# Performance work log

Hardware: AMD Instinct MI355X
Metric: run time of the kernel (lower is better)

## Reference

```python
import jax, jax.numpy as jnp
import numpy as np

B, CIN, COUT, H, W = 2, 256, 256, 96, 96
K, PAD, G = 3, 1, 4           # kernel, padding, deformable_groups
KK = K * K
CG = CIN // G                 # channels per deformable group


def setup_inputs() -> dict:
    key = jax.random.key(0)
    k1, k2, k3, k4 = jax.random.split(key, 4)
    feature = jax.random.normal(k1, (B, CIN, H, W), jnp.float32)
    pred_shape = jax.random.normal(k2, (B, H * W, 4), jnp.float32)
    # init_weights: normal(std=0.01), no biases
    w_offset = jax.random.normal(k3, (G * KK * 2, 4, 1, 1), jnp.float32) * 0.01
    w_deform = jax.random.normal(k4, (COUT, CIN, K, K), jnp.float32) * 0.01
    return {"feature": feature, "pred_shape": pred_shape,
            "w_offset": w_offset, "w_deform": w_deform}


def reference(feature, pred_shape, w_offset, w_deform):
    # pred_shape: (B, H*W, 4) -> (B, 4, H, W); detached in the original
    ps = jnp.transpose(pred_shape, (0, 2, 1)).reshape(B, -1, H, W)
    ps = jax.lax.stop_gradient(ps)
    # 1x1 offset conv: (B, G*2*KK, H, W)
    offset = jnp.einsum('bchw,oc->bohw', ps, w_offset[:, :, 0, 0])
    # mmcv layout per group: [y_k0, x_k0, y_k1, x_k1, ...]
    off = offset.reshape(B, G, KK, 2, H, W)
    off_y, off_x = off[:, :, :, 0], off[:, :, :, 1]   # (B, G, KK, H, W)

    kk = jnp.arange(KK)
    ky = (kk // K).reshape(KK, 1, 1).astype(jnp.float32)
    kx = (kk % K).reshape(KK, 1, 1).astype(jnp.float32)
    yy = jnp.arange(H, dtype=jnp.float32).reshape(1, H, 1)
    xx = jnp.arange(W, dtype=jnp.float32).reshape(1, 1, W)
    # sampling positions (stride=1, dilation=1): (B, G, KK, H, W)
    py = (yy - PAD + ky)[None, None] + off_y
    px = (xx - PAD + kx)[None, None] + off_x

    img = feature.reshape(B, G, CG, H * W)

    def gather(yi, xi):
        # zero outside the image (matches DCN bilinear with zero padding)
        valid = ((yi >= 0) & (yi < H) & (xi >= 0) & (xi < W)).astype(feature.dtype)
        idx = jnp.clip(yi, 0, H - 1) * W + jnp.clip(xi, 0, W - 1)
        v = jnp.take_along_axis(img, idx.reshape(B, G, 1, KK * H * W), axis=3)
        return v.reshape(B, G, CG, KK, H, W) * valid[:, :, None]

    y0 = jnp.floor(py); x0 = jnp.floor(px)
    ly = py - y0; lx = px - x0
    y0i = y0.astype(jnp.int32); x0i = x0.astype(jnp.int32)

    val = ((1 - ly) * (1 - lx))[:, :, None] * gather(y0i, x0i) \
        + ((1 - ly) * lx)[:, :, None] * gather(y0i, x0i + 1) \
        + (ly * (1 - lx))[:, :, None] * gather(y0i + 1, x0i) \
        + (ly * lx)[:, :, None] * gather(y0i + 1, x0i + 1)

    sampled = val.reshape(B, CIN, KK, H, W)
    out = jnp.einsum('bckhw,ock->bohw', sampled, w_deform.reshape(COUT, CIN, KK))
    return jax.nn.relu(out)
```

## Files before the change

### kernel.cpp

```cpp
#include <hip/hip_runtime.h>
#include <hip/hip_bf16.h>
#include <stdint.h>

#define HH   96
#define WW   96
#define HW   9216
#define CIN  256
#define COUT 256
#define NB   2
#define NG   4
#define CG   64
#define KK   9
#define KTOT 2304
#define KB   288
#define TS   8
#define WIN  12
#define W2   13
#define SCH  32

typedef __attribute__((ext_vector_type(8))) short short8;
typedef __attribute__((ext_vector_type(4))) float f32x4;
typedef __attribute__((ext_vector_type(4))) uint32_t u32x4;

__device__ __forceinline__ uint32_t pk2bf(float v0, float v1) {
    __hip_bfloat162 h = __float22bfloat162_rn(make_float2(v0, v1));
    uint32_t u;
    __builtin_memcpy(&u, &h, 4);
    return u;
}

__global__ __launch_bounds__(256) void prep_A(const float* __restrict__ wd,
                                              uint16_t* __restrict__ Ablk) {
    int t  = blockIdx.x * 256 + threadIdx.x;
    int kb = t % KB;
    int o  = t / KB;
    int kkA = kb >> 5;
    int c0A = (kb & 31) * 8;
    const float* src = wd + (size_t)o * KTOT + c0A * KK + kkA;
    float a[8];
#pragma unroll
    for (int e = 0; e < 8; ++e) a[e] = src[e * KK];
    uint16_t* dst = Ablk + ((size_t)kb * 256 + o) * 8;
    u32x4 v;
    v.x = pk2bf(a[0], a[1]);
    v.y = pk2bf(a[2], a[3]);
    v.z = pk2bf(a[4], a[5]);
    v.w = pk2bf(a[6], a[7]);
    *(u32x4*)dst = v;
}

__global__ __launch_bounds__(256) void sampler(const float* __restrict__ feature,
                                               const float* __restrict__ pred,
                                               const float* __restrict__ woff,
                                               uint16_t* __restrict__ S) {
    __shared__ float2 ft2[(SCH / 2) * WIN * W2];

    int tid = threadIdx.x;
    int cb = blockIdx.y, b = blockIdx.z;
    int ch0 = cb * SCH;
    int g = ch0 >> 6;
    int ty = blockIdx.x / (WW / TS), tx = blockIdx.x % (WW / TS);
    int r0 = ty * TS, c0 = tx * TS;
    int rlo = min(max(r0 - 2, 0), HH - WIN);
    int clo = min(max(c0 - 2, 0), WW - WIN);
    bool interior = (rlo >= 1) && (rlo + WIN <= HH - 1) &&
                    (clo >= 1) && (clo + WIN <= WW - 1);

    float* ftf = (float*)ft2;
    const float* fg = feature + ((size_t)(b * CIN + ch0)) * HW;
    for (int e = tid; e < SCH * WIN * WIN; e += 256) {
        int ch = e / (WIN * WIN);
        int re = e - ch * (WIN * WIN);
        int rr = re / WIN, cc = re - rr * WIN;
        ftf[(ch >> 1) * (WIN * W2 * 2) + (rr * W2 + cc) * 2 + (ch & 1)] =
            fg[(size_t)ch * HW + (rlo + rr) * WW + clo + cc];
    }
    __syncthreads();

    int lane = tid & 63, wv = tid >> 6;
    int lr = lane >> 3, lc = lane & 7;
    int hy = r0 + lr, hx = c0 + lc;
    int p = hy * WW + hx;
    float4 ps4 = *(const float4*)(pred + ((size_t)b * HW + p) * 4);

    const float2* ftw = ft2 + (wv * 4) * (WIN * W2);
    const float* fgw = fg + (size_t)(wv * 8) * HW;
    int kb_base = cb * 4 + wv;

#pragma unroll
    for (int kk = 0; kk < KK; ++kk) {
        const float* wy = woff + (g * KK + kk) * 8;
        float offy = ps4.x * wy[0] + ps4.y * wy[1] + ps4.z * wy[2] + ps4.w * wy[3];
        float offx = ps4.x * wy[4] + ps4.y * wy[5] + ps4.z * wy[6] + ps4.w * wy[7];
        float py = (float)(hy - 1 + kk / 3) + offy;
        float px = (float)(hx - 1 + kk % 3) + offx;
        float fy = floorf(py), fx = floorf(px);
        int y0 = (int)fy, x0 = (int)fx;
        float ly = py - fy, lx = px - fx;

        uint16_t* Sp = S + (((size_t)b * KB + (kk * 32 + kb_base)) * HW + p) * 8;
        uint32_t pk[4];

        float c00, c01, c10, c11;
        bool fast;
        int r, q;
        if (interior) {
            fast = (y0 >= rlo) & (y0 <= rlo + WIN - 2) &
                   (x0 >= clo) & (x0 <= clo + WIN - 2);
            if (fast) {
                c00 = (1.f - ly) * (1.f - lx); c01 = (1.f - ly) * lx;
                c10 = ly * (1.f - lx);         c11 = ly * lx;
                r = y0; q = x0;
            } else {
                r = min(max(y0, 0), HH - 2);
                q = min(max(x0, 0), WW - 2);
                float wyA = (y0 == r) ? (1.f - ly) : ((y0 == -1) ? ly : 0.f);
                float wyB = (y0 == r) ? ly : ((y0 == HH - 1) ? (1.f - ly) : 0.f);
                float wxA = (x0 == q) ? (1.f - lx) : ((x0 == -1) ? lx : 0.f);
                float wxB = (x0 == q) ? lx : ((x0 == WW - 1) ? (1.f - lx) : 0.f);
                c00 = wyA * wxA; c01 = wyA * wxB;
                c10 = wyB * wxA; c11 = wyB * wxB;
            }
        } else {
            r = min(max(y0, 0), HH - 2);
            q = min(max(x0, 0), WW - 2);
            float wyA = (y0 == r) ? (1.f - ly) : ((y0 == -1) ? ly : 0.f);
            float wyB = (y0 == r) ? ly : ((y0 == HH - 1) ? (1.f - ly) : 0.f);
            float wxA = (x0 == q) ? (1.f - lx) : ((x0 == -1) ? lx : 0.f);
            float wxB = (x0 == q) ? lx : ((x0 == WW - 1) ? (1.f - lx) : 0.f);
            c00 = wyA * wxA; c01 = wyA * wxB;
            c10 = wyB * wxA; c11 = wyB * wxB;
            fast = (r >= rlo) & (r <= rlo + WIN - 2) &
                   (q >= clo) & (q <= clo + WIN - 2);
        }

        if (fast) {
            int base = (r - rlo) * W2 + (q - clo);
#pragma unroll
            for (int ep = 0; ep < 4; ++ep) {
                const float2* f0 = ftw + ep * (WIN * W2) + base;
                float2 p00 = f0[0], p01 = f0[1];
                float2 p10 = f0[W2], p11 = f0[W2 + 1];
                float v0 = c00 * p00.x + c01 * p01.x + c10 * p10.x + c11 * p11.x;
                float v1 = c00 * p00.y + c01 * p01.y + c10 * p10.y + c11 * p11.y;
                pk[ep] = pk2bf(v0, v1);
            }
        } else {
            size_t gb = (size_t)r * WW + q;
#pragma unroll
            for (int ep = 0; ep < 4; ++ep) {
                const float* f0 = fgw + (size_t)(2 * ep) * HW + gb;
                const float* f1 = f0 + HW;
                float v0 = c00 * f0[0] + c01 * f0[1] + c10 * f0[WW] + c11 * f0[WW + 1];
                float v1 = c00 * f1[0] + c01 * f1[1] + c10 * f1[WW] + c11 * f1[WW + 1];
                pk[ep] = pk2bf(v0, v1);
            }
        }
        u32x4 vv = {pk[0], pk[1], pk[2], pk[3]};
        *(u32x4*)(Sp) = vv;
    }
}

__global__ __launch_bounds__(64, 2) void gemm_kernel(const uint16_t* __restrict__ S,
                                                     const uint16_t* __restrict__ Ablk,
                                                     float* __restrict__ out) {
    int lane = threadIdx.x;
    int bid = blockIdx.x;
    int xcd = bid & 7;
    int j   = bid >> 3;
    int my  = j & 3;
    int pairid = xcd * 36 + (j >> 2);
    int b  = pairid / 144;
    int py = pairid % 144;
    int o0 = my * 64, col0 = py * 64;
    int kc = lane >> 4, il = lane & 15;

    const uint16_t* Ap = Ablk + ((size_t)kc * 256 + o0 + il) * 8;
    const uint16_t* Bp = S + (size_t)b * KB * HW * 8 + ((size_t)kc * HW + col0 + il) * 8;
    const size_t Astep = (size_t)4 * 256 * 8;
    const size_t Bstep = (size_t)4 * HW * 8;

    f32x4 acc[4][4];
#pragma unroll
    for (int m = 0; m < 4; ++m)
#pragma unroll
        for (int n = 0; n < 4; ++n) acc[m][n] = (f32x4){0.f, 0.f, 0.f, 0.f};

    const int NT = KTOT / 32;

    short8 a0[4], b0[4], a1[4], b1[4];

#define LOADT(t, areg, breg)                                                   \
    {                                                                          \
        const uint16_t* ap = Ap + (size_t)(t) * Astep;                         \
        const uint16_t* bp = Bp + (size_t)(t) * Bstep;                         \
        areg[0] = *(const short8*)(ap + 0 * 16 * 8);                           \
        areg[1] = *(const short8*)(ap + 1 * 16 * 8);                           \
        areg[2] = *(const short8*)(ap + 2 * 16 * 8);                           \
        areg[3] = *(const short8*)(ap + 3 * 16 * 8);                           \
        breg[0] = *(const short8*)(bp + 0 * 16 * 8);                           \
        breg[1] = *(const short8*)(bp + 1 * 16 * 8);                           \
        breg[2] = *(const short8*)(bp + 2 * 16 * 8);                           \
        breg[3] = *(const short8*)(bp + 3 * 16 * 8);                           \
    }

#define MFMAT(areg, breg)                                                      \
    {                                                                          \
        _Pragma("unroll")                                                      \
        for (int m = 0; m < 4; ++m)                                            \
            _Pragma("unroll")                                                  \
            for (int n = 0; n < 4; ++n)                                        \
                acc[m][n] = __builtin_amdgcn_mfma_f32_16x16x32_bf16(           \
                    areg[m], breg[n], acc[m][n], 0, 0, 0);                     \
    }

    LOADT(0, a0, b0);
    LOADT(1, a1, b1);

    for (int tt = 0; tt < NT; tt += 2) {
        MFMAT(a0, b0);
        if (tt + 2 < NT) LOADT(tt + 2, a0, b0);
        MFMAT(a1, b1);
        if (tt + 3 < NT) LOADT(tt + 3, a1, b1);
    }
#undef LOADT
#undef MFMAT

    int r4 = kc * 4;
    size_t obase = ((size_t)b * COUT + o0) * HW + col0;
#pragma unroll
    for (int m = 0; m < 4; ++m)
#pragma unroll
        for (int n = 0; n < 4; ++n)
#pragma unroll
            for (int r = 0; r < 4; ++r) {
                float v = acc[m][n][r];
                v = v > 0.f ? v : 0.f;
                out[obase + (size_t)(m * 16 + r4 + r) * HW + n * 16 + il] = v;
            }
}

extern "C" void kernel_launch(void* const* d_in, const int* in_sizes, int n_in,
                              void* d_out, int out_size, void* d_ws, size_t ws_size,
                              hipStream_t stream) {
    (void)in_sizes; (void)n_in; (void)out_size; (void)ws_size;
    const float* feature = (const float*)d_in[0];
    const float* pred    = (const float*)d_in[1];
    const float* woff    = (const float*)d_in[2];
    const float* wdef    = (const float*)d_in[3];
    float* out = (float*)d_out;

    const size_t S_BYTES = (size_t)NB * KB * HW * 8 * 2;
    uint16_t* S    = (uint16_t*)d_ws;
    uint16_t* Ablk = (uint16_t*)((char*)d_ws + S_BYTES);

    hipLaunchKernelGGL(prep_A, dim3(288), dim3(256), 0, stream, wdef, Ablk);
    hipLaunchKernelGGL(sampler, dim3((HH / TS) * (WW / TS), CIN / SCH, NB), dim3(256), 0, stream,
                       feature, pred, woff, S);
    hipLaunchKernelGGL(gemm_kernel, dim3(1152), dim3(64), 0, stream,
                       S, Ablk, out);
}
```

Before: 77.83 us.

## Split GEMM K-loop across two waves with LDS reduction; plain float sampler tile

The GEMM kernel now launches two waves per block. Each wave handles half of the K dimension, wave 1 passes its accumulators to wave 0 through shared memory, and wave 0 adds them, applies ReLU and writes the output. The aim is to double the waves in flight per output tile and hide more memory latency. The cost is extra LDS traffic, a block-wide barrier, and an epilogue with one wave idle. Separately, the sampler's shared tile changes from channel-pair interleaved float2 to a plain per-channel float layout, so each bilinear tap uses two scalar LDS loads instead of one float2 load.

Result: no change. 77.86 us (+0.0%).

```diff
diff --git a/kernel.cpp b/kernel.cpp
--- a/kernel.cpp
+++ b/kernel.cpp
@@ -53,7 +53,7 @@
                                                const float* __restrict__ pred,
                                                const float* __restrict__ woff,
                                                uint16_t* __restrict__ S) {
-    __shared__ float2 ft2[(SCH / 2) * WIN * W2];
+    __shared__ float ft[SCH * WIN * W2];
 
     int tid = threadIdx.x;
     int cb = blockIdx.y, b = blockIdx.z;
@@ -66,13 +66,12 @@
     bool interior = (rlo >= 1) && (rlo + WIN <= HH - 1) &&
                     (clo >= 1) && (clo + WIN <= WW - 1);
 
-    float* ftf = (float*)ft2;
     const float* fg = feature + ((size_t)(b * CIN + ch0)) * HW;
     for (int e = tid; e < SCH * WIN * WIN; e += 256) {
         int ch = e / (WIN * WIN);
         int re = e - ch * (WIN * WIN);
         int rr = re / WIN, cc = re - rr * WIN;
-        ftf[(ch >> 1) * (WIN * W2 * 2) + (rr * W2 + cc) * 2 + (ch & 1)] =
+        ft[ch * (WIN * W2) + rr * W2 + cc] =
             fg[(size_t)ch * HW + (rlo + rr) * WW + clo + cc];
     }
     __syncthreads();
@@ -83,7 +82,7 @@
     int p = hy * WW + hx;
     float4 ps4 = *(const float4*)(pred + ((size_t)b * HW + p) * 4);
 
-    const float2* ftw = ft2 + (wv * 4) * (WIN * W2);
+    const float* ftw = ft + (wv * 8) * (WIN * W2);
     const float* fgw = fg + (size_t)(wv * 8) * HW;
     int kb_base = cb * 4 + wv;
 
@@ -138,11 +137,10 @@
             int base = (r - rlo) * W2 + (q - clo);
 #pragma unroll
             for (int ep = 0; ep < 4; ++ep) {
-                const float2* f0 = ftw + ep * (WIN * W2) + base;
-                float2 p00 = f0[0], p01 = f0[1];
-                float2 p10 = f0[W2], p11 = f0[W2 + 1];
-                float v0 = c00 * p00.x + c01 * p01.x + c10 * p10.x + c11 * p11.x;
-                float v1 = c00 * p00.y + c01 * p01.y + c10 * p10.y + c11 * p11.y;
+                const float* f0 = ftw + (2 * ep) * (WIN * W2) + base;
+                const float* f1 = f0 + (WIN * W2);
+                float v0 = c00 * f0[0] + c01 * f0[1] + c10 * f0[W2] + c11 * f0[W2 + 1];
+                float v1 = c00 * f1[0] + c01 * f1[1] + c10 * f1[W2] + c11 * f1[W2 + 1];
                 pk[ep] = pk2bf(v0, v1);
             }
         } else {
@@ -161,10 +159,13 @@
     }
 }
 
-__global__ __launch_bounds__(64, 2) void gemm_kernel(const uint16_t* __restrict__ S,
-                                                     const uint16_t* __restrict__ Ablk,
-                                                     float* __restrict__ out) {
-    int lane = threadIdx.x;
+__global__ __launch_bounds__(128, 2) void gemm_kernel(const uint16_t* __restrict__ S,
+                                                      const uint16_t* __restrict__ Ablk,
+                                                      float* __restrict__ out) {
+    __shared__ f32x4 sh[16][64];
+
+    int tid = threadIdx.x;
+    int lane = tid & 63, wv = tid >> 6;
     int bid = blockIdx.x;
     int xcd = bid & 7;
     int j   = bid >> 3;
@@ -175,18 +176,19 @@
     int o0 = my * 64, col0 = py * 64;
     int kc = lane >> 4, il = lane & 15;
 
-    const uint16_t* Ap = Ablk + ((size_t)kc * 256 + o0 + il) * 8;
-    const uint16_t* Bp = S + (size_t)b * KB * HW * 8 + ((size_t)kc * HW + col0 + il) * 8;
     const size_t Astep = (size_t)4 * 256 * 8;
     const size_t Bstep = (size_t)4 * HW * 8;
+    const int HT = KTOT / 32 / 2;
+
+    const uint16_t* Ap = Ablk + ((size_t)kc * 256 + o0 + il) * 8 + (size_t)wv * HT * Astep;
+    const uint16_t* Bp = S + (size_t)b * KB * HW * 8 + ((size_t)kc * HW + col0 + il) * 8
+                           + (size_t)wv * HT * Bstep;
 
     f32x4 acc[4][4];
 #pragma unroll
     for (int m = 0; m < 4; ++m)
 #pragma unroll
         for (int n = 0; n < 4; ++n) acc[m][n] = (f32x4){0.f, 0.f, 0.f, 0.f};
-
-    const int NT = KTOT / 32;
 
     short8 a0[4], b0[4], a1[4], b1[4];
 
@@ -217,27 +219,39 @@
     LOADT(0, a0, b0);
     LOADT(1, a1, b1);
 
-    for (int tt = 0; tt < NT; tt += 2) {
+    for (int tt = 0; tt < HT; tt += 2) {
         MFMAT(a0, b0);
-        if (tt + 2 < NT) LOADT(tt + 2, a0, b0);
+        if (tt + 2 < HT) LOADT(tt + 2, a0, b0);
         MFMAT(a1, b1);
-        if (tt + 3 < NT) LOADT(tt + 3, a1, b1);
+        if (tt + 3 < HT) LOADT(tt + 3, a1, b1);
     }
 #undef LOADT
 #undef MFMAT
 
-    int r4 = kc * 4;
-    size_t obase = ((size_t)b * COUT + o0) * HW + col0;
-#pragma unroll
-    for (int m = 0; m < 4; ++m)
-#pragma unroll
-        for (int n = 0; n < 4; ++n)
-#pragma unroll
-            for (int r = 0; r < 4; ++r) {
-                float v = acc[m][n][r];
-                v = v > 0.f ? v : 0.f;
-                out[obase + (size_t)(m * 16 + r4 + r) * HW + n * 16 + il] = v;
-            }
+    if (wv == 1) {
+#pragma unroll
+        for (int m = 0; m < 4; ++m)
+#pragma unroll
+            for (int n = 0; n < 4; ++n)
+                sh[m * 4 + n][lane] = acc[m][n];
+    }
+    __syncthreads();
+    if (wv == 0) {
+        int r4 = kc * 4;
+        size_t obase = ((size_t)b * COUT + o0) * HW + col0;
+#pragma unroll
+        for (int m = 0; m < 4; ++m)
+#pragma unroll
+            for (int n = 0; n < 4; ++n) {
+                f32x4 s2 = sh[m * 4 + n][lane];
+#pragma unroll
+                for (int r = 0; r < 4; ++r) {
+                    float v = acc[m][n][r] + s2[r];
+                    v = v > 0.f ? v : 0.f;
+                    out[obase + (size_t)(m * 16 + r4 + r) * HW + n * 16 + il] = v;
+                }
+            }
+    }
 }
 
 extern "C" void kernel_launch(void* const* d_in, const int* in_sizes, int n_in,
@@ -257,6 +271,6 @@
     hipLaunchKernelGGL(prep_A, dim3(288), dim3(256), 0, stream, wdef, Ablk);
     hipLaunchKernelGGL(sampler, dim3((HH / TS) * (WW / TS), CIN / SCH, NB), dim3(256), 0, stream,
                        feature, pred, woff, S);
-    hipLaunchKernelGGL(gemm_kernel, dim3(1152), dim3(64), 0, stream,
+    hipLaunchKernelGGL(gemm_kernel, dim3(1152), dim3(128), 0, stream,
                        S, Ablk, out);
 }
```
